# Optimization experiments

Hardware: AMD Instinct MI355X
Metric: run time of the kernel (lower is better)

Reference implementation:

```python
import jax, jax.numpy as jnp
import numpy as np

VOCAB = 50257
HIDDEN = [1024, 512]
NUM_CLASSES = 20


def setup_inputs() -> dict:
    key = jax.random.key(0)
    ks = jax.random.split(key, 8)
    B, S = 1024, 512
    x = jax.random.randint(ks[0], (B, S), 0, VOCAB, dtype=jnp.int32)
    def lin(kw, kb, fan_in, fan_out):
        lim = 1.0 / np.sqrt(fan_in)
        W = jax.random.uniform(kw, (fan_in, fan_out), minval=-lim, maxval=lim, dtype=jnp.float32)
        b = jax.random.uniform(kb, (fan_out,), minval=-lim, maxval=lim, dtype=jnp.float32)
        return W, b
    W1, b1 = lin(ks[1], ks[2], VOCAB, HIDDEN[0])
    W2, b2 = lin(ks[3], ks[4], HIDDEN[0], HIDDEN[1])
    Wout, bout = lin(ks[5], ks[6], HIDDEN[1], NUM_CLASSES)
    return {"x": x, "W1": W1, "b1": b1, "W2": W2, "b2": b2, "Wout": Wout, "bout": bout}


def bow_counts(x, vocab):
    # Fused batched histogram: scatter-add of ones into a flat [B*V] buffer.
    B = x.shape[0]
    flat = (jnp.arange(B, dtype=x.dtype)[:, None] * vocab + x).reshape(-1)
    bow = jnp.zeros((B * vocab,), dtype=jnp.float32).at[flat].add(1.0)
    return bow.reshape(B, vocab)


def reference(x, W1, b1, W2, b2, Wout, bout):
    bow = bow_counts(x, VOCAB)                       # [B, V]
    h = jax.nn.relu(bow @ W1 + b1)                   # [B, 1024]
    h = jax.nn.relu(h @ W2 + b2)                     # [B, 512]  (dropout = identity at inference)
    return h @ Wout + bout                           # [B, num_classes]
```

## Files before the change

kernel.cpp:

```cpp
#include <hip/hip_runtime.h>

#define VOCAB 50257
#define BATCH 1024
#define SEQ   512
#define H1    1024
#define H2    512
#define NC    20

typedef float floatx4 __attribute__((ext_vector_type(4)));

#define NRANGE 128
#define RNGW   393
#define NSTEP  (NRANGE / 8)
#define RPB    8
#define NRT    (BATCH / RPB)
#define CAPR   128
#define CAPP   (CAPR + 8)

__global__ __launch_bounds__(256) void k1_range(
    const int* __restrict__ x, const float* __restrict__ W1,
    float* __restrict__ px) {
    const int b   = blockIdx.x;
    const int xcd = b & 7;
    const int rt  = b >> 3;
    const int r0  = rt * RPB;
    const int tid = threadIdx.x;

    __shared__ int cnt[NSTEP];
    __shared__ int lists[NSTEP][CAPP];

    if (tid < NSTEP) cnt[tid] = 0;
    __syncthreads();

#pragma unroll 4
    for (int k = 0; k < RPB * SEQ / 256; ++k) {
        const int j = k * 256 + tid;
        const int t = __builtin_nontemporal_load(&x[(size_t)r0 * SEQ + j]);
        const int rng = t / RNGW;
        if ((rng & 7) == xcd) {
            const int idx = atomicAdd(&cnt[rng >> 3], 1);
            if (idx < CAPR) lists[rng >> 3][idx] = ((j >> 9) << 16) | t;
        }
    }
    __syncthreads();
    if (tid < NSTEP) {
        const int n    = min(cnt[tid], CAPR);
        const int npad = (n + 7) & ~7;
        for (int i = n; i < npad; ++i) lists[tid][i] = 8 << 16;
    }
    __syncthreads();

    floatx4 a0 = (floatx4)0.f, a1 = (floatx4)0.f, a2 = (floatx4)0.f,
            a3 = (floatx4)0.f, a4 = (floatx4)0.f, a5 = (floatx4)0.f,
            a6 = (floatx4)0.f, a7 = (floatx4)0.f;

#define RFL(v)  __builtin_amdgcn_readfirstlane(v)
#define LDW(e)  (*((const floatx4*)(W1 + (size_t)((e) & 0xFFFF) * H1) + tid))
#define ACC(e, w)                                                            \
    do {                                                                     \
        switch ((e) >> 16) {                                                 \
            case 0: a0 += (w); break;                                        \
            case 1: a1 += (w); break;                                        \
            case 2: a2 += (w); break;                                        \
            case 3: a3 += (w); break;                                        \
            case 4: a4 += (w); break;                                        \
            case 5: a5 += (w); break;                                        \
            case 6: a6 += (w); break;                                        \
            case 7: a7 += (w); break;                                        \
            default: break;                                                  \
        }                                                                    \
    } while (0)

    for (int step = 0; step < NSTEP; ++step) {
        const int n = RFL(min(cnt[step], CAPR));
        if (n == 0) continue;
        const int ng = (n + 7) >> 3;
        const int* lp = lists[step];

        int e0 = RFL(lp[0]), e1 = RFL(lp[1]), e2 = RFL(lp[2]), e3 = RFL(lp[3]),
            e4 = RFL(lp[4]), e5 = RFL(lp[5]), e6 = RFL(lp[6]), e7 = RFL(lp[7]);
        floatx4 w0 = LDW(e0), w1 = LDW(e1), w2 = LDW(e2), w3 = LDW(e3),
                w4 = LDW(e4), w5 = LDW(e5), w6 = LDW(e6), w7 = LDW(e7);

        for (int g = 0; g + 1 < ng; ++g) {
            const int* lq = lp + (g + 1) * 8;
            const int f0 = RFL(lq[0]), f1 = RFL(lq[1]), f2 = RFL(lq[2]),
                      f3 = RFL(lq[3]), f4 = RFL(lq[4]), f5 = RFL(lq[5]),
                      f6 = RFL(lq[6]), f7 = RFL(lq[7]);
            const floatx4 v0 = LDW(f0), v1 = LDW(f1), v2 = LDW(f2),
                          v3 = LDW(f3), v4 = LDW(f4), v5 = LDW(f5),
                          v6 = LDW(f6), v7 = LDW(f7);
            ACC(e0, w0); ACC(e1, w1); ACC(e2, w2); ACC(e3, w3);
            ACC(e4, w4); ACC(e5, w5); ACC(e6, w6); ACC(e7, w7);
            e0 = f0; e1 = f1; e2 = f2; e3 = f3;
            e4 = f4; e5 = f5; e6 = f6; e7 = f7;
            w0 = v0; w1 = v1; w2 = v2; w3 = v3;
            w4 = v4; w5 = v5; w6 = v6; w7 = v7;
        }
        ACC(e0, w0); ACC(e1, w1); ACC(e2, w2); ACC(e3, w3);
        ACC(e4, w4); ACC(e5, w5); ACC(e6, w6); ACC(e7, w7);
    }
#undef ACC
#undef LDW
#undef RFL

    floatx4* dst = (floatx4*)(px + ((size_t)xcd * BATCH + r0) * H1) + tid;
    __builtin_nontemporal_store(a0, dst + 0 * (H1 / 4));
    __builtin_nontemporal_store(a1, dst + 1 * (H1 / 4));
    __builtin_nontemporal_store(a2, dst + 2 * (H1 / 4));
    __builtin_nontemporal_store(a3, dst + 3 * (H1 / 4));
    __builtin_nontemporal_store(a4, dst + 4 * (H1 / 4));
    __builtin_nontemporal_store(a5, dst + 5 * (H1 / 4));
    __builtin_nontemporal_store(a6, dst + 6 * (H1 / 4));
    __builtin_nontemporal_store(a7, dst + 7 * (H1 / 4));
}

__global__ __launch_bounds__(256) void k1b_reduce(
    const float* __restrict__ px, float* __restrict__ p) {
    const size_t i4 = (size_t)blockIdx.x * 256 + threadIdx.x;
    const floatx4* s = (const floatx4*)px + i4;
    floatx4 a = __builtin_nontemporal_load(s);
#pragma unroll
    for (int xc = 1; xc < 8; ++xc)
        a += __builtin_nontemporal_load(s + (size_t)xc * BATCH * (H1 / 4));
    ((floatx4*)p)[i4] = a;
}

template<int SSPLIT>
__global__ __launch_bounds__(256) void k1_gather(
    const int* __restrict__ x, const float* __restrict__ W1,
    float* __restrict__ p) {
    const int row = blockIdx.x / SSPLIT;
    const int s   = blockIdx.x % SSPLIT;
    const int tid = threadIdx.x;
    constexpr int TOK = SEQ / SSPLIT;

    __shared__ int toks[TOK];
    for (int i = tid; i < TOK; i += 256) toks[i] = x[row * SEQ + s * TOK + i];
    __syncthreads();

    floatx4 acc = (floatx4)0.f;
#pragma unroll 8
    for (int t = 0; t < TOK; ++t)
        acc += ((const floatx4*)(W1 + (size_t)toks[t] * H1))[tid];
    ((floatx4*)p)[((size_t)s * BATCH + row) * (H1 / 4) + tid] = acc;
}

template<int NPART>
__global__ __launch_bounds__(256) void k2_gemm(
    const float* __restrict__ p, const float* __restrict__ b1,
    const float* __restrict__ W2, const float* __restrict__ b2,
    float* __restrict__ h2) {
    __shared__ float As[16][H1];
    const int tid = threadIdx.x;
    const int rt  = blockIdx.x >> 2;
    const int ct  = blockIdx.x & 3;
    const int r0  = rt * 16;

    const float* __restrict__ p1 = p + (size_t)BATCH * H1;

    for (int i = tid; i < 16 * (H1 / 4); i += 256) {
        const int r  = i >> 8;
        const int k4 = i & 255;
        float4 v = ((const float4*)(p + ((size_t)(r0 + r)) * H1))[k4];
        if (NPART == 2) {
            const float4 u = ((const float4*)(p1 + ((size_t)(r0 + r)) * H1))[k4];
            v.x += u.x; v.y += u.y; v.z += u.z; v.w += u.w;
        }
        const float4 bb = ((const float4*)b1)[k4];
        As[r][k4 * 4 + 0] = fmaxf(v.x + bb.x, 0.f);
        As[r][k4 * 4 + 1] = fmaxf(v.y + bb.y, 0.f);
        As[r][k4 * 4 + 2] = fmaxf(v.z + bb.z, 0.f);
        As[r][k4 * 4 + 3] = fmaxf(v.w + bb.w, 0.f);
    }
    __syncthreads();

    const int q  = tid & 31;
    const int ks = tid >> 5;

    float4 acc[16];
#pragma unroll
    for (int r = 0; r < 16; ++r) acc[r] = make_float4(0.f, 0.f, 0.f, 0.f);

    const float* __restrict__ w2base = W2 + (size_t)ct * 128 + q * 4;
#pragma unroll 2
    for (int kk = 0; kk < 128; ++kk) {
        const int k = ks * 128 + kk;
        const float4 w = *(const float4*)(w2base + (size_t)k * H2);
#pragma unroll
        for (int r = 0; r < 16; ++r) {
            const float a = As[r][k];
            acc[r].x += a * w.x; acc[r].y += a * w.y;
            acc[r].z += a * w.z; acc[r].w += a * w.w;
        }
    }

    __syncthreads();
    float4* Rs = (float4*)As;
#define RS(rs, r) Rs[(((rs) * 32 + q) * 16) + (r)]
    if (ks >= 4) {
#pragma unroll
        for (int r = 0; r < 16; ++r) RS(ks - 4, r) = acc[r];
    }
    __syncthreads();
    if (ks < 4) {
#pragma unroll
        for (int r = 0; r < 16; ++r) {
            const float4 t = RS(ks, r);
            acc[r].x += t.x; acc[r].y += t.y; acc[r].z += t.z; acc[r].w += t.w;
        }
    }
    __syncthreads();
    if (ks == 2 || ks == 3) {
#pragma unroll
        for (int r = 0; r < 16; ++r) RS(ks - 2, r) = acc[r];
    }
    __syncthreads();
    if (ks < 2) {
#pragma unroll
        for (int r = 0; r < 16; ++r) {
            const float4 t = RS(ks, r);
            acc[r].x += t.x; acc[r].y += t.y; acc[r].z += t.z; acc[r].w += t.w;
        }
    }
    __syncthreads();
    if (ks == 1) {
#pragma unroll
        for (int r = 0; r < 16; ++r) RS(0, r) = acc[r];
    }
    __syncthreads();
    if (ks == 0) {
        const float4 bb = *(const float4*)(b2 + ct * 128 + q * 4);
#pragma unroll
        for (int r = 0; r < 16; ++r) {
            const float4 t = RS(0, r);
            float4 o;
            o.x = fmaxf(acc[r].x + t.x + bb.x, 0.f);
            o.y = fmaxf(acc[r].y + t.y + bb.y, 0.f);
            o.z = fmaxf(acc[r].z + t.z + bb.z, 0.f);
            o.w = fmaxf(acc[r].w + t.w + bb.w, 0.f);
            *(float4*)(h2 + (size_t)(r0 + r) * H2 + ct * 128 + q * 4) = o;
        }
    }
#undef RS
}

__global__ __launch_bounds__(256) void k3_out(
    const float* __restrict__ h2, const float* __restrict__ Wout,
    const float* __restrict__ bout, float* __restrict__ out) {
    const int gid = blockIdx.x * 256 + threadIdx.x;
    const int r = gid >> 5;
    const int c = gid & 31;
    if (c >= NC) return;

    float acc = bout[c];
    const float* __restrict__ hrow = h2 + (size_t)r * H2;
#pragma unroll 8
    for (int k = 0; k < H2; ++k)
        acc += hrow[k] * Wout[k * NC + c];
    out[r * NC + c] = acc;
}

extern "C" void kernel_launch(void* const* d_in, const int* in_sizes, int n_in,
                              void* d_out, int out_size, void* d_ws, size_t ws_size,
                              hipStream_t stream) {
    const int*   x    = (const int*)d_in[0];
    const float* W1   = (const float*)d_in[1];
    const float* b1   = (const float*)d_in[2];
    const float* W2   = (const float*)d_in[3];
    const float* b2   = (const float*)d_in[4];
    const float* Wout = (const float*)d_in[5];
    const float* bout = (const float*)d_in[6];
    float* out = (float*)d_out;

    const size_t needA = ((size_t)8 * BATCH * H1 + (size_t)BATCH * H1 +
                          (size_t)BATCH * H2) * 4;
    const size_t need2 = ((size_t)2 * BATCH * H1 + (size_t)BATCH * H2) * 4;

    if (ws_size >= needA) {
        float* px = (float*)d_ws;
        float* p  = px + (size_t)8 * BATCH * H1;
        float* h2 = p + (size_t)BATCH * H1;
        k1_range<<<8 * NRT, 256, 0, stream>>>(x, W1, px);
        k1b_reduce<<<BATCH * H1 / 4 / 256, 256, 0, stream>>>(px, p);
        k2_gemm<1><<<256, 256, 0, stream>>>(p, b1, W2, b2, h2);
        k3_out<<<BATCH * 32 / 256, 256, 0, stream>>>(h2, Wout, bout, out);
    } else if (ws_size >= need2) {
        float* p  = (float*)d_ws;
        float* h2 = p + (size_t)2 * BATCH * H1;
        k1_gather<2><<<BATCH * 2, 256, 0, stream>>>(x, W1, p);
        k2_gemm<2><<<256, 256, 0, stream>>>(p, b1, W2, b2, h2);
        k3_out<<<BATCH * 32 / 256, 256, 0, stream>>>(h2, Wout, bout, out);
    } else {
        float* p  = (float*)d_ws;
        float* h2 = p + (size_t)BATCH * H1;
        k1_gather<1><<<BATCH, 256, 0, stream>>>(x, W1, p);
        k2_gemm<1><<<256, 256, 0, stream>>>(p, b1, W2, b2, h2);
        k3_out<<<BATCH * 32 / 256, 256, 0, stream>>>(h2, Wout, bout, out);
    }
}
```

Measured before the change: 238.4 us.

## Flatten per-range token lists into one prefix-summed list and halve rows per block

The range kernel now bins tokens into a single flat shared list using a count pass, a prefix sum and a fill pass, instead of fixed-capacity per-step lists that were padded separately. The gather loop then runs once over the whole padded list rather than once per step, which removes per-step padding and loop overhead. Rows per block drop from 8 to 4, doubling the block count and cutting accumulator registers. In exchange there is an extra pass over shared tokens, a serial prefix sum on one thread, and a flat capacity limit that could silently drop tokens if a block's count ever exceeds it.

```diff
diff --git a/kernel.cpp b/kernel.cpp
--- a/kernel.cpp
+++ b/kernel.cpp
@@ -12,10 +12,11 @@
 #define NRANGE 128
 #define RNGW   393
 #define NSTEP  (NRANGE / 8)
-#define RPB    8
+#define RPB    4
+#define TPB    (RPB * SEQ)
 #define NRT    (BATCH / RPB)
-#define CAPR   128
-#define CAPP   (CAPR + 8)
+#define FLATCAP 448
+#define SENT   (RPB << 16)
 
 __global__ __launch_bounds__(256) void k1_range(
     const int* __restrict__ x, const float* __restrict__ W1,
@@ -26,33 +27,52 @@
     const int r0  = rt * RPB;
     const int tid = threadIdx.x;
 
-    __shared__ int cnt[NSTEP];
-    __shared__ int lists[NSTEP][CAPP];
-
-    if (tid < NSTEP) cnt[tid] = 0;
-    __syncthreads();
-
-#pragma unroll 4
-    for (int k = 0; k < RPB * SEQ / 256; ++k) {
+    __shared__ int toks[TPB];
+    __shared__ int flat[FLATCAP];
+    __shared__ int cnt[NSTEP], pref[NSTEP], fill[NSTEP];
+    __shared__ int tot_s;
+
+    if (tid < NSTEP) { cnt[tid] = 0; fill[tid] = 0; }
+    __syncthreads();
+
+#pragma unroll
+    for (int k = 0; k < TPB / 256; ++k) {
         const int j = k * 256 + tid;
         const int t = __builtin_nontemporal_load(&x[(size_t)r0 * SEQ + j]);
+        toks[j] = t;
+        const int rng = t / RNGW;
+        if ((rng & 7) == xcd) atomicAdd(&cnt[rng >> 3], 1);
+    }
+    __syncthreads();
+
+    if (tid == 0) {
+        int s = 0;
+#pragma unroll
+        for (int i = 0; i < NSTEP; ++i) { pref[i] = s; s += cnt[i]; }
+        tot_s = s;
+    }
+    __syncthreads();
+
+#pragma unroll
+    for (int k = 0; k < TPB / 256; ++k) {
+        const int j = k * 256 + tid;
+        const int t = toks[j];
         const int rng = t / RNGW;
         if ((rng & 7) == xcd) {
-            const int idx = atomicAdd(&cnt[rng >> 3], 1);
-            if (idx < CAPR) lists[rng >> 3][idx] = ((j >> 9) << 16) | t;
-        }
-    }
-    __syncthreads();
-    if (tid < NSTEP) {
-        const int n    = min(cnt[tid], CAPR);
-        const int npad = (n + 7) & ~7;
-        for (int i = n; i < npad; ++i) lists[tid][i] = 8 << 16;
-    }
-    __syncthreads();
-
-    floatx4 a0 = (floatx4)0.f, a1 = (floatx4)0.f, a2 = (floatx4)0.f,
-            a3 = (floatx4)0.f, a4 = (floatx4)0.f, a5 = (floatx4)0.f,
-            a6 = (floatx4)0.f, a7 = (floatx4)0.f;
+            const int pos = pref[rng >> 3] + atomicAdd(&fill[rng >> 3], 1);
+            if (pos < FLATCAP) flat[pos] = ((j >> 9) << 16) | t;
+        }
+    }
+    __syncthreads();
+    {
+        const int tot  = tot_s;
+        const int npad = (tot + 7) & ~7;
+        if (tid < npad - tot) flat[tot + tid] = SENT;
+    }
+    __syncthreads();
+
+    floatx4 a0 = (floatx4)0.f, a1 = (floatx4)0.f,
+            a2 = (floatx4)0.f, a3 = (floatx4)0.f;
 
 #define RFL(v)  __builtin_amdgcn_readfirstlane(v)
 #define LDW(e)  (*((const floatx4*)(W1 + (size_t)((e) & 0xFFFF) * H1) + tid))
@@ -63,19 +83,14 @@
             case 1: a1 += (w); break;                                        \
             case 2: a2 += (w); break;                                        \
             case 3: a3 += (w); break;                                        \
-            case 4: a4 += (w); break;                                        \
-            case 5: a5 += (w); break;                                        \
-            case 6: a6 += (w); break;                                        \
-            case 7: a7 += (w); break;                                        \
             default: break;                                                  \
         }                                                                    \
     } while (0)
 
-    for (int step = 0; step < NSTEP; ++step) {
-        const int n = RFL(min(cnt[step], CAPR));
-        if (n == 0) continue;
-        const int ng = (n + 7) >> 3;
-        const int* lp = lists[step];
+    const int ntot = RFL((tot_s + 7) & ~7);
+    if (ntot > 0) {
+        const int ng = ntot >> 3;
+        const int* lp = flat;
 
         int e0 = RFL(lp[0]), e1 = RFL(lp[1]), e2 = RFL(lp[2]), e3 = RFL(lp[3]),
             e4 = RFL(lp[4]), e5 = RFL(lp[5]), e6 = RFL(lp[6]), e7 = RFL(lp[7]);
@@ -109,10 +124,6 @@
     __builtin_nontemporal_store(a1, dst + 1 * (H1 / 4));
     __builtin_nontemporal_store(a2, dst + 2 * (H1 / 4));
     __builtin_nontemporal_store(a3, dst + 3 * (H1 / 4));
-    __builtin_nontemporal_store(a4, dst + 4 * (H1 / 4));
-    __builtin_nontemporal_store(a5, dst + 5 * (H1 / 4));
-    __builtin_nontemporal_store(a6, dst + 6 * (H1 / 4));
-    __builtin_nontemporal_store(a7, dst + 7 * (H1 / 4));
 }
 
 __global__ __launch_bounds__(256) void k1b_reduce(
```

New measurement: 277.1 us. +16.3%, slower.
